# Kernel tuning notes

Measured on AMD Instinct MI355X. Metric: run time of the kernel, lower is better.

## Reference

```python
import jax, jax.numpy as jnp
import numpy as np

N = 50000          # nodes
E = 800000         # edges (before self loops)
H = 4              # attention heads
C = 64             # per-head channels
D_IN = 256
NEG_ATT = 0.2      # GATConv attention LeakyReLU slope
NEG_ACT = 0.01     # nn.LeakyReLU default slope
EPS = 1e-5
MLP_DIMS = [64, 32, 16, 2]


def _gat_layer(x, src, dst, W, a_src, a_dst, b, concat):
    """PyG GATConv: gather -> segment-softmax over dst -> scatter-add."""
    n = x.shape[0]
    h = (x @ W).reshape(n, H, C)                       # [N,H,C]
    s = (h * a_src).sum(-1)                            # [N,H]
    d = (h * a_dst).sum(-1)                            # [N,H]
    e = jax.nn.leaky_relu(s[src] + d[dst], NEG_ATT)    # [E',H]
    m = jax.ops.segment_max(e, dst, num_segments=n)    # per-dst max (self loops -> no empty segs)
    w = jnp.exp(e - m[dst])
    den = jax.ops.segment_sum(w, dst, num_segments=n)
    alpha = w / den[dst]                               # [E',H]
    out = jax.ops.segment_sum(alpha[:, :, None] * h[src], dst, num_segments=n)  # [N,H,C]
    out = out.reshape(n, H * C) if concat else out.mean(axis=1)
    return out + b


def _graph_norm(x, w, b, a):
    mu = x.mean(axis=0, keepdims=True)
    y = x - a * mu
    var = (y * y).mean(axis=0, keepdims=True)
    return w * y * jax.lax.rsqrt(var + EPS) + b


def setup_inputs() -> dict:
    key = jax.random.key(0)
    ks = jax.random.split(key, 40)
    d = {
        'x': jax.random.normal(ks[0], (N, D_IN), dtype=jnp.float32),
        'edge_index': jax.random.randint(ks[1], (2, E), 0, N, dtype=jnp.int64),
    }
    dims_in = [D_IN, H * C, H * C]
    norm_dims = [H * C, H * C, C]
    k = 2
    for i in range(3):
        fan = dims_in[i]
        d[f'W{i}'] = jax.random.normal(ks[k], (fan, H * C), dtype=jnp.float32) / np.sqrt(fan); k += 1
        d[f'as{i}'] = jax.random.normal(ks[k], (H, C), dtype=jnp.float32) / np.sqrt(C); k += 1
        d[f'ad{i}'] = jax.random.normal(ks[k], (H, C), dtype=jnp.float32) / np.sqrt(C); k += 1
        d[f'b{i}'] = jnp.zeros((norm_dims[i],), dtype=jnp.float32)
        d[f'gw{i}'] = jnp.ones((norm_dims[i],), dtype=jnp.float32)
        d[f'gb{i}'] = jnp.zeros((norm_dims[i],), dtype=jnp.float32)
        d[f'ga{i}'] = jnp.ones((norm_dims[i],), dtype=jnp.float32)
    for j in range(3):
        fi, fo = MLP_DIMS[j], MLP_DIMS[j + 1]
        d[f'mW{j}'] = jax.random.normal(ks[k], (fi, fo), dtype=jnp.float32) / np.sqrt(fi); k += 1
        d[f'mb{j}'] = jnp.zeros((fo,), dtype=jnp.float32)
    return d


def reference(x, edge_index,
              W0, as0, ad0, b0, gw0, gb0, ga0,
              W1, as1, ad1, b1, gw1, gb1, ga1,
              W2, as2, ad2, b2, gw2, gb2, ga2,
              mW0, mb0, mW1, mb1, mW2, mb2):
    n = x.shape[0]
    loop = jnp.arange(n, dtype=edge_index.dtype)
    src = jnp.concatenate([edge_index[0], loop])   # add self loops (PyG default)
    dst = jnp.concatenate([edge_index[1], loop])

    h = _gat_layer(x, src, dst, W0, as0, ad0, b0, concat=True)
    h = jax.nn.leaky_relu(_graph_norm(h, gw0, gb0, ga0), NEG_ACT)
    h = _gat_layer(h, src, dst, W1, as1, ad1, b1, concat=True)
    h = jax.nn.leaky_relu(_graph_norm(h, gw1, gb1, ga1), NEG_ACT)
    h = _gat_layer(h, src, dst, W2, as2, ad2, b2, concat=False)
    h = jax.nn.leaky_relu(_graph_norm(h, gw2, gb2, ga2), NEG_ACT)

    h = jax.nn.relu(h @ mW0 + mb0)
    h = jax.nn.relu(h @ mW1 + mb1)
    return h @ mW2 + mb2
```

## Files before the change

kernel.cpp:

```cpp
#include <hip/hip_runtime.h>

#define NN 50000
#define EE 800000
#define ET 850000
#define HH 4
#define CC 64
#define FDIM 256

#define SCAN_BLK 512
#define SCAN_NB ((NN + SCAN_BLK - 1) / SCAN_BLK)

typedef unsigned short ushort;
typedef __bf16 bf16x8 __attribute__((ext_vector_type(8)));
typedef float floatx4 __attribute__((ext_vector_type(4)));
typedef ushort ushort8v __attribute__((ext_vector_type(8)));
struct ushort4s { ushort x, y, z, w; };

__device__ __forceinline__ ushort f2bf(float f) {
  union { float f; unsigned u; } v; v.f = f;
  unsigned r = v.u + 0x7fffu + ((v.u >> 16) & 1u);
  return (ushort)(r >> 16);
}
__device__ __forceinline__ float bf2f(ushort u) {
  return __uint_as_float(((unsigned)u) << 16);
}

__device__ __forceinline__ int get_edge(const void* p, int is64, long long idx) {
  if (is64) return (int)((const long long*)p)[idx];
  return ((const int*)p)[idx];
}

__global__ void detect_kernel(const unsigned int* p, int* flag) {
  __shared__ unsigned red[256];
  int t = threadIdx.x;
  unsigned o = 0;
  for (int i = 0; i < 4; i++) o |= p[(t * 4 + i) * 2 + 1];
  red[t] = o;
  __syncthreads();
  for (int s = 128; s > 0; s >>= 1) {
    if (t < s) red[t] |= red[t + s];
    __syncthreads();
  }
  if (t == 0) *flag = (red[0] == 0) ? 1 : 0;
}

__global__ void degree_kernel(const void* eidx, const int* flag, int* deg) {
  int k = blockIdx.x * blockDim.x + threadIdx.x;
  if (k >= ET) return;
  int is64 = *flag;
  int dst = (k < EE) ? get_edge(eidx, is64, (long long)EE + k) : (k - EE);
  atomicAdd(&deg[dst], 1);
}

__global__ __launch_bounds__(SCAN_BLK) void scan1_kernel(const int* __restrict__ deg,
                                                         int* __restrict__ rowptr,
                                                         int* __restrict__ bsum) {
  __shared__ int sm[SCAN_BLK];
  int t = threadIdx.x;
  int i = blockIdx.x * SCAN_BLK + t;
  int v = (i < NN) ? deg[i] : 0;
  sm[t] = v;
  __syncthreads();
#pragma unroll
  for (int o = 1; o < SCAN_BLK; o <<= 1) {
    int u = (t >= o) ? sm[t - o] : 0;
    __syncthreads();
    sm[t] += u;
    __syncthreads();
  }
  if (i < NN) rowptr[i] = sm[t] - v;
  if (t == SCAN_BLK - 1) bsum[blockIdx.x] = sm[t];
}

__global__ __launch_bounds__(128) void scan2_kernel(const int* __restrict__ bsum,
                                                    int* __restrict__ boff,
                                                    int* __restrict__ rowptr) {
  __shared__ int sm[128];
  int t = threadIdx.x;
  int v = (t < SCAN_NB) ? bsum[t] : 0;
  sm[t] = v;
  __syncthreads();
#pragma unroll
  for (int o = 1; o < 128; o <<= 1) {
    int u = (t >= o) ? sm[t - o] : 0;
    __syncthreads();
    sm[t] += u;
    __syncthreads();
  }
  if (t < SCAN_NB) boff[t] = sm[t] - v;
  if (t == 0) rowptr[NN] = ET;
}

__global__ __launch_bounds__(SCAN_BLK) void scan3_kernel(int* __restrict__ rowptr,
                                                         int* __restrict__ cursor,
                                                         const int* __restrict__ boff) {
  int i = blockIdx.x * SCAN_BLK + threadIdx.x;
  if (i >= NN) return;
  int v = rowptr[i] + boff[blockIdx.x];
  rowptr[i] = v;
  cursor[i] = v;
}

__global__ void fill_kernel(const void* eidx, const int* flag, int* cursor, int* csr_src) {
  int k = blockIdx.x * blockDim.x + threadIdx.x;
  if (k >= ET) return;
  int is64 = *flag;
  int src, dst;
  if (k < EE) {
    src = get_edge(eidx, is64, k);
    dst = get_edge(eidx, is64, (long long)EE + k);
  } else {
    src = dst = k - EE;
  }
  int pos = atomicAdd(&cursor[dst], 1);
  csr_src[pos] = src;
}

__global__ void conv_w_kernel(const float* __restrict__ W0, const float* __restrict__ W1,
                              const float* __restrict__ W2,
                              ushort* __restrict__ T0, ushort* __restrict__ T1,
                              ushort* __restrict__ T2) {
  const float* W = (blockIdx.y == 0) ? W0 : (blockIdx.y == 1) ? W1 : W2;
  ushort* Wt = (blockIdx.y == 0) ? T0 : (blockIdx.y == 1) ? T1 : T2;
  int idx = blockIdx.x * 256 + threadIdx.x;
  int k = idx >> 8, n = idx & 255;
  Wt[n * 256 + k] = f2bf(W[idx]);
}

template <int MODE>
__global__ __launch_bounds__(256) void gemm_bf16(const void* __restrict__ Ap,
                                                 const ushort* __restrict__ Bt,
                                                 ushort* __restrict__ C,
                                                 const float* __restrict__ as_,
                                                 const float* __restrict__ ad_,
                                                 float* __restrict__ s_arr,
                                                 float* __restrict__ d_arr,
                                                 const float* __restrict__ colsum,
                                                 const float* __restrict__ colsumsq,
                                                 const float* __restrict__ ga,
                                                 const float* __restrict__ gw,
                                                 const float* __restrict__ gb) {
  __shared__ ushort As[4 * 512];
  __shared__ ushort Bs[8 * 512];
  __shared__ float scs[FDIM], shs[FDIM];
  int tid = threadIdx.x, w = tid >> 6, l = tid & 63;
  int brow0 = blockIdx.x * 64, bcol0 = blockIdx.y * 128;
  int lm = l & 15, lk = (l >> 4) * 8;
  int arA = min(brow0 + w * 16 + lm, NN - 1);
  size_t arowA = (size_t)arA * 256 + lk;
  const ushort* bg0 = Bt + (size_t)(bcol0 + (2 * w) * 16 + lm) * 256 + lk;
  const ushort* bg1 = Bt + (size_t)(bcol0 + (2 * w + 1) * 16 + lm) * 256 + lk;

  if constexpr (MODE == 1) {
    const float invn = 1.0f / (float)NN;
    float mu = colsum[tid] * invn;
    float ex2 = colsumsq[tid] * invn;
    float a = ga[tid];
    float var = fmaxf(ex2 - (2.f * a - a * a) * mu * mu, 0.f);
    float s = gw[tid] * rsqrtf(var + 1e-5f);
    scs[tid] = s;
    shs[tid] = gb[tid] - s * a * mu;
    __syncthreads();
  }

  floatx4 acc[2][4];
#pragma unroll
  for (int i = 0; i < 2; i++)
#pragma unroll
    for (int j = 0; j < 4; j++) acc[i][j] = floatx4{0.f, 0.f, 0.f, 0.f};

  int wm = (w >> 1) * 2, wn = (w & 1) * 4;

  for (int k0 = 0; k0 < 256; k0 += 32) {
    ushort8v a0;
    if constexpr (MODE == 0) {
      const float* p0 = (const float*)Ap + arowA + k0;
      float4 u0 = *(const float4*)p0, v0 = *(const float4*)(p0 + 4);
      a0 = ushort8v{f2bf(u0.x), f2bf(u0.y), f2bf(u0.z), f2bf(u0.w),
                    f2bf(v0.x), f2bf(v0.y), f2bf(v0.z), f2bf(v0.w)};
    } else {
      ushort8v r0 = *(const ushort8v*)((const ushort*)Ap + arowA + k0);
      int kb = k0 + lk;
#pragma unroll
      for (int j = 0; j < 8; j++) {
        float sc = scs[kb + j], sh = shs[kb + j];
        float y0 = fmaf(sc, bf2f(r0[j]), sh);
        y0 = fmaxf(y0, 0.01f * y0);
        a0[j] = f2bf(y0);
      }
    }
    ushort8v b0 = *(const ushort8v*)(bg0 + k0);
    ushort8v b1 = *(const ushort8v*)(bg1 + k0);
    *(ushort8v*)&As[w * 512 + l * 8] = a0;
    *(ushort8v*)&Bs[(2 * w) * 512 + l * 8] = b0;
    *(ushort8v*)&Bs[(2 * w + 1) * 512 + l * 8] = b1;
    __syncthreads();
    bf16x8 af[2], bfr[4];
#pragma unroll
    for (int i = 0; i < 2; i++) af[i] = *(const bf16x8*)&As[(wm + i) * 512 + l * 8];
#pragma unroll
    for (int j = 0; j < 4; j++) bfr[j] = *(const bf16x8*)&Bs[(wn + j) * 512 + l * 8];
#pragma unroll
    for (int i = 0; i < 2; i++)
#pragma unroll
      for (int j = 0; j < 4; j++)
        acc[i][j] = __builtin_amdgcn_mfma_f32_16x16x32_bf16(af[i], bfr[j], acc[i][j], 0, 0, 0);
    __syncthreads();
  }

  int quad = l >> 4;
#pragma unroll
  for (int i = 0; i < 2; i++) {
    int r0 = brow0 + (wm + i) * 16 + quad * 4;
#pragma unroll
    for (int j = 0; j < 4; j++) {
      int col = bcol0 + (wn + j) * 16 + lm;
#pragma unroll
      for (int r = 0; r < 4; r++) {
        int row = r0 + r;
        if (row < NN) C[(size_t)row * 256 + col] = f2bf(acc[i][j][r]);
      }
    }
  }
  float asv[4], adv[4];
#pragma unroll
  for (int j = 0; j < 4; j++) {
    int col = bcol0 + (wn + j) * 16 + lm;
    asv[j] = as_[col];
    adv[j] = ad_[col];
  }
  int head = (bcol0 >> 6) + (w & 1);
#pragma unroll
  for (int i = 0; i < 2; i++) {
#pragma unroll
    for (int r = 0; r < 4; r++) {
      float sp = acc[i][0][r] * asv[0] + acc[i][1][r] * asv[1] +
                 acc[i][2][r] * asv[2] + acc[i][3][r] * asv[3];
      float dp = acc[i][0][r] * adv[0] + acc[i][1][r] * adv[1] +
                 acc[i][2][r] * adv[2] + acc[i][3][r] * adv[3];
      sp += __shfl_xor(sp, 1); dp += __shfl_xor(dp, 1);
      sp += __shfl_xor(sp, 2); dp += __shfl_xor(dp, 2);
      sp += __shfl_xor(sp, 4); dp += __shfl_xor(dp, 4);
      sp += __shfl_xor(sp, 8); dp += __shfl_xor(dp, 8);
      if (lm == 0) {
        int row = brow0 + (wm + i) * 16 + quad * 4 + r;
        if (row < NN) {
          s_arr[row * HH + head] = sp;
          d_arr[row * HH + head] = dp;
        }
      }
    }
  }
}

template <bool CONCAT>
__global__ __launch_bounds__(256) void agg_kernel(const ushort* __restrict__ hb,
                                                  const float* __restrict__ s_arr,
                                                  const float* __restrict__ d_arr,
                                                  const int* __restrict__ rowptr,
                                                  const int* __restrict__ csr_src,
                                                  const float* __restrict__ bias,
                                                  void* __restrict__ outp) {
  int w = __builtin_amdgcn_readfirstlane(threadIdx.x >> 6);
  int l = threadIdx.x & 63;
  int head = l >> 4;
  int n = blockIdx.x * 4 + w;
  int beg = rowptr[n], end = rowptr[n + 1];
  float dh = d_arr[n * HH + head];
  float a0 = 0.f, a1 = 0.f, a2 = 0.f, a3 = 0.f, den = 0.f;

  int i = beg;
  for (; i + 16 <= end; i += 16) {
    int ss[16];
#pragma unroll
    for (int t = 0; t < 16; t++) ss[t] = csr_src[i + t];
    float ee[16];
#pragma unroll
    for (int t = 0; t < 16; t++) ee[t] = s_arr[ss[t] * HH + head];
    ushort4s hh[16];
#pragma unroll
    for (int t = 0; t < 16; t++)
      hh[t] = *(const ushort4s*)(hb + (unsigned)(ss[t] * FDIM + l * 4));
#pragma unroll
    for (int t = 0; t < 16; t++) {
      float e = ee[t] + dh;
      e = (e > 0.f) ? e : 0.2f * e;
      float wt = __expf(e);
      den += wt;
      a0 = fmaf(wt, bf2f(hh[t].x), a0);
      a1 = fmaf(wt, bf2f(hh[t].y), a1);
      a2 = fmaf(wt, bf2f(hh[t].z), a2);
      a3 = fmaf(wt, bf2f(hh[t].w), a3);
    }
  }
  for (; i + 8 <= end; i += 8) {
    int ss[8];
#pragma unroll
    for (int t = 0; t < 8; t++) ss[t] = csr_src[i + t];
    float ee[8];
#pragma unroll
    for (int t = 0; t < 8; t++) ee[t] = s_arr[ss[t] * HH + head];
    ushort4s hh[8];
#pragma unroll
    for (int t = 0; t < 8; t++)
      hh[t] = *(const ushort4s*)(hb + (unsigned)(ss[t] * FDIM + l * 4));
#pragma unroll
    for (int t = 0; t < 8; t++) {
      float e = ee[t] + dh;
      e = (e > 0.f) ? e : 0.2f * e;
      float wt = __expf(e);
      den += wt;
      a0 = fmaf(wt, bf2f(hh[t].x), a0);
      a1 = fmaf(wt, bf2f(hh[t].y), a1);
      a2 = fmaf(wt, bf2f(hh[t].z), a2);
      a3 = fmaf(wt, bf2f(hh[t].w), a3);
    }
  }
  for (; i + 4 <= end; i += 4) {
    int ss[4];
#pragma unroll
    for (int t = 0; t < 4; t++) ss[t] = csr_src[i + t];
    float ee[4];
#pragma unroll
    for (int t = 0; t < 4; t++) ee[t] = s_arr[ss[t] * HH + head];
    ushort4s hh[4];
#pragma unroll
    for (int t = 0; t < 4; t++)
      hh[t] = *(const ushort4s*)(hb + (unsigned)(ss[t] * FDIM + l * 4));
#pragma unroll
    for (int t = 0; t < 4; t++) {
      float e = ee[t] + dh;
      e = (e > 0.f) ? e : 0.2f * e;
      float wt = __expf(e);
      den += wt;
      a0 = fmaf(wt, bf2f(hh[t].x), a0);
      a1 = fmaf(wt, bf2f(hh[t].y), a1);
      a2 = fmaf(wt, bf2f(hh[t].z), a2);
      a3 = fmaf(wt, bf2f(hh[t].w), a3);
    }
  }
  for (; i < end; i++) {
    int s0 = csr_src[i];
    float e0 = s_arr[s0 * HH + head] + dh;
    ushort4s h0 = *(const ushort4s*)(hb + (unsigned)(s0 * FDIM + l * 4));
    e0 = (e0 > 0.f) ? e0 : 0.2f * e0;
    float w0 = __expf(e0);
    den += w0;
    a0 = fmaf(w0, bf2f(h0.x), a0); a1 = fmaf(w0, bf2f(h0.y), a1);
    a2 = fmaf(w0, bf2f(h0.z), a2); a3 = fmaf(w0, bf2f(h0.w), a3);
  }
  float inv = 1.0f / den;
  float r0 = a0 * inv, r1 = a1 * inv, r2 = a2 * inv, r3 = a3 * inv;

  if (CONCAT) {
    float4 bv = ((const float4*)bias)[l];
    ushort4s o;
    o.x = f2bf(r0 + bv.x); o.y = f2bf(r1 + bv.y);
    o.z = f2bf(r2 + bv.z); o.w = f2bf(r3 + bv.w);
    ((ushort4s*)outp)[(unsigned)(n * 64 + l)] = o;
  } else {
    r0 += __shfl_xor(r0, 16); r1 += __shfl_xor(r1, 16);
    r2 += __shfl_xor(r2, 16); r3 += __shfl_xor(r3, 16);
    r0 += __shfl_xor(r0, 32); r1 += __shfl_xor(r1, 32);
    r2 += __shfl_xor(r2, 32); r3 += __shfl_xor(r3, 32);
    if (l < 16) {
      float4 bv = ((const float4*)bias)[l];
      float4 o;
      o.x = 0.25f * r0 + bv.x; o.y = 0.25f * r1 + bv.y;
      o.z = 0.25f * r2 + bv.z; o.w = 0.25f * r3 + bv.w;
      ((float4*)outp)[(unsigned)(n * 16 + l)] = o;
    }
  }
}

__global__ __launch_bounds__(256) void norm_reduce_bf(const ushort* __restrict__ xin,
                                                      float* colsum, float* colsumsq) {
  __shared__ float4 sm1[256], sm2[256];
  int t = threadIdx.x;
  int c4 = (t & 63) * 4;
  int rl = t >> 6;
  int r0 = blockIdx.x * 128;
  int r1 = min(NN, r0 + 128);
  float s0 = 0.f, s1 = 0.f, s2 = 0.f, s3 = 0.f;
  float q0 = 0.f, q1 = 0.f, q2 = 0.f, q3 = 0.f;
  for (int r = r0 + rl; r < r1; r += 4) {
    ushort4s v = *(const ushort4s*)(xin + (size_t)r * FDIM + c4);
    float f0 = bf2f(v.x), f1 = bf2f(v.y), f2 = bf2f(v.z), f3 = bf2f(v.w);
    s0 += f0; q0 += f0 * f0;
    s1 += f1; q1 += f1 * f1;
    s2 += f2; q2 += f2 * f2;
    s3 += f3; q3 += f3 * f3;
  }
  sm1[t] = float4{s0, s1, s2, s3};
  sm2[t] = float4{q0, q1, q2, q3};
  __syncthreads();
  if (t < 64) {
    float4 a = sm1[t], b = sm1[t + 64], c = sm1[t + 128], d = sm1[t + 192];
    atomicAdd(&colsum[c4 + 0], a.x + b.x + c.x + d.x);
    atomicAdd(&colsum[c4 + 1], a.y + b.y + c.y + d.y);
    atomicAdd(&colsum[c4 + 2], a.z + b.z + c.z + d.z);
    atomicAdd(&colsum[c4 + 3], a.w + b.w + c.w + d.w);
    float4 e = sm2[t], f = sm2[t + 64], g = sm2[t + 128], h = sm2[t + 192];
    atomicAdd(&colsumsq[c4 + 0], e.x + f.x + g.x + h.x);
    atomicAdd(&colsumsq[c4 + 1], e.y + f.y + g.y + h.y);
    atomicAdd(&colsumsq[c4 + 2], e.z + f.z + g.z + h.z);
    atomicAdd(&colsumsq[c4 + 3], e.w + f.w + g.w + h.w);
  }
}

__global__ __launch_bounds__(256) void norm_reduce_f32(const float* __restrict__ xin,
                                                       float* colsum, float* colsumsq) {
  int f = threadIdx.x & (CC - 1);
  int rl = threadIdx.x / CC;
  int r0 = blockIdx.x * 128;
  int r1 = min(NN, r0 + 128);
  float s1 = 0.f, s2 = 0.f;
  for (int r = r0 + rl; r < r1; r += 4) {
    float v = xin[(size_t)r * CC + f];
    s1 += v; s2 += v * v;
  }
  atomicAdd(&colsum[f], s1);
  atomicAdd(&colsumsq[f], s2);
}

__global__ __launch_bounds__(256) void mlp_kernel(const float* __restrict__ xin,
                                                  const float* __restrict__ colsum,
                                                  const float* __restrict__ colsumsq,
                                                  const float* __restrict__ ga,
                                                  const float* __restrict__ gw,
                                                  const float* __restrict__ gb,
                                                  const float* mW0, const float* mb0,
                                                  const float* mW1, const float* mb1,
                                                  const float* mW2, const float* mb2,
                                                  float* __restrict__ out) {
  __shared__ float W0s[64 * 32];
  __shared__ float W1s[32 * 16];
  __shared__ float W2s[16 * 2];
  __shared__ float b0s[32], b1s[16], b2s[2];
  __shared__ float sc[CC], sh[CC];
  int t = threadIdx.x;
  for (int i = t; i < 2048; i += 256) W0s[i] = mW0[i];
  for (int i = t; i < 512; i += 256) W1s[i] = mW1[i];
  if (t < 32) { W2s[t] = mW2[t]; b0s[t] = mb0[t]; }
  if (t < 16) b1s[t] = mb1[t];
  if (t < 2) b2s[t] = mb2[t];
  if (t < CC) {
    const float invn = 1.0f / (float)NN;
    float mu = colsum[t] * invn;
    float ex2 = colsumsq[t] * invn;
    float a = ga[t];
    float var = fmaxf(ex2 - (2.f * a - a * a) * mu * mu, 0.f);
    float s = gw[t] * rsqrtf(var + 1e-5f);
    sc[t] = s; sh[t] = gb[t] - s * a * mu;
  }
  __syncthreads();
  int node = blockIdx.x * 256 + t;
  if (node >= NN) return;
  float in[64];
  const float* xr = xin + (size_t)node * 64;
#pragma unroll
  for (int k = 0; k < 64; k++) {
    float y = sc[k] * xr[k] + sh[k];
    in[k] = (y > 0.f) ? y : 0.01f * y;
  }
  float h1[32];
#pragma unroll
  for (int j = 0; j < 32; j++) h1[j] = b0s[j];
#pragma unroll
  for (int k = 0; k < 64; k++) {
    float v = in[k];
#pragma unroll
    for (int j = 0; j < 32; j++) h1[j] += v * W0s[k * 32 + j];
  }
#pragma unroll
  for (int j = 0; j < 32; j++) h1[j] = fmaxf(h1[j], 0.f);
  float h2[16];
#pragma unroll
  for (int j = 0; j < 16; j++) h2[j] = b1s[j];
#pragma unroll
  for (int k = 0; k < 32; k++) {
    float v = h1[k];
#pragma unroll
    for (int j = 0; j < 16; j++) h2[j] += v * W1s[k * 16 + j];
  }
#pragma unroll
  for (int j = 0; j < 16; j++) h2[j] = fmaxf(h2[j], 0.f);
  float o0 = b2s[0], o1 = b2s[1];
#pragma unroll
  for (int k = 0; k < 16; k++) {
    o0 += h2[k] * W2s[k * 2 + 0];
    o1 += h2[k] * W2s[k * 2 + 1];
  }
  out[(size_t)node * 2 + 0] = o0;
  out[(size_t)node * 2 + 1] = o1;
}

extern "C" void kernel_launch(void* const* d_in, const int* in_sizes, int n_in,
                              void* d_out, int out_size, void* d_ws, size_t ws_size,
                              hipStream_t stream) {
  const float* x = (const float*)d_in[0];
  const void* ei = d_in[1];
  const float* W[3]   = {(const float*)d_in[2],  (const float*)d_in[9],  (const float*)d_in[16]};
  const float* as_[3] = {(const float*)d_in[3],  (const float*)d_in[10], (const float*)d_in[17]};
  const float* ad_[3] = {(const float*)d_in[4],  (const float*)d_in[11], (const float*)d_in[18]};
  const float* b_[3]  = {(const float*)d_in[5],  (const float*)d_in[12], (const float*)d_in[19]};
  const float* gw[3]  = {(const float*)d_in[6],  (const float*)d_in[13], (const float*)d_in[20]};
  const float* gb[3]  = {(const float*)d_in[7],  (const float*)d_in[14], (const float*)d_in[21]};
  const float* ga[3]  = {(const float*)d_in[8],  (const float*)d_in[15], (const float*)d_in[22]};
  const float* mW0 = (const float*)d_in[23];
  const float* mb0 = (const float*)d_in[24];
  const float* mW1 = (const float*)d_in[25];
  const float* mb1 = (const float*)d_in[26];
  const float* mW2 = (const float*)d_in[27];
  const float* mb2 = (const float*)d_in[28];
  float* out = (float*)d_out;

  char* ws = (char*)d_ws;
  size_t off = 0;
  auto take = [&](size_t bytes) -> char* {
    char* p = ws + off;
    off = (off + bytes + 255) & ~(size_t)255;
    return p;
  };
  ushort* hb    = (ushort*)take((size_t)NN * FDIM * 2);
  ushort* aggb  = (ushort*)take((size_t)NN * FDIM * 2);
  float* bufD   = (float*)take((size_t)NN * CC * 4);
  ushort* Wt[3];
  for (int i = 0; i < 3; i++) Wt[i] = (ushort*)take((size_t)256 * 256 * 2);
  float* s_arr  = (float*)take((size_t)NN * HH * 4);
  float* d_arr  = (float*)take((size_t)NN * HH * 4);
  char* zbase   = (char*)take(0);
  int* deg      = (int*)take((size_t)NN * 4);
  float* cs[3];
  for (int i = 0; i < 3; i++) cs[i] = (float*)take(2048);
  size_t zlen   = (size_t)(((char*)cs[2] + 2048) - zbase);
  int* cursor   = (int*)take((size_t)NN * 4);
  int* rowptr   = (int*)take((size_t)(NN + 1) * 4);
  int* csr_src  = (int*)take((size_t)ET * 4);
  int* bsum     = (int*)take(512);
  int* boff     = (int*)take(512);
  int* flag     = (int*)take(256);

  hipMemsetAsync(zbase, 0, zlen, stream);

  detect_kernel<<<1, 256, 0, stream>>>((const unsigned int*)ei, flag);
  degree_kernel<<<(ET + 255) / 256, 256, 0, stream>>>(ei, flag, deg);
  scan1_kernel<<<SCAN_NB, SCAN_BLK, 0, stream>>>(deg, rowptr, bsum);
  scan2_kernel<<<1, 128, 0, stream>>>(bsum, boff, rowptr);
  scan3_kernel<<<SCAN_NB, SCAN_BLK, 0, stream>>>(rowptr, cursor, boff);
  fill_kernel<<<(ET + 255) / 256, 256, 0, stream>>>(ei, flag, cursor, csr_src);

  conv_w_kernel<<<dim3(256, 3), 256, 0, stream>>>(W[0], W[1], W[2], Wt[0], Wt[1], Wt[2]);

  dim3 ggrid((NN + 63) / 64, 2);
  for (int L = 0; L < 3; L++) {
    if (L == 0)
      gemm_bf16<0><<<ggrid, 256, 0, stream>>>((const void*)x, Wt[0], hb,
                                              as_[0], ad_[0], s_arr, d_arr,
                                              nullptr, nullptr, nullptr, nullptr, nullptr);
    else
      gemm_bf16<1><<<ggrid, 256, 0, stream>>>((const void*)aggb, Wt[L], hb,
                                              as_[L], ad_[L], s_arr, d_arr,
                                              cs[L - 1], cs[L - 1] + 256,
                                              ga[L - 1], gw[L - 1], gb[L - 1]);
    if (L < 2) {
      agg_kernel<true><<<NN / 4, 256, 0, stream>>>(hb, s_arr, d_arr, rowptr, csr_src, b_[L], aggb);
      norm_reduce_bf<<<(NN + 127) / 128, 256, 0, stream>>>(aggb, cs[L], cs[L] + 256);
    } else {
      agg_kernel<false><<<NN / 4, 256, 0, stream>>>(hb, s_arr, d_arr, rowptr, csr_src, b_[L], bufD);
      norm_reduce_f32<<<(NN + 127) / 128, 256, 0, stream>>>(bufD, cs[2], cs[2] + 256);
    }
  }
  mlp_kernel<<<(NN + 255) / 256, 256, 0, stream>>>(bufD, cs[2], cs[2] + 256,
                                                   ga[2], gw[2], gb[2],
                                                   mW0, mb0, mW1, mb1, mW2, mb2, out);
}
```

Measured before the change: 686.2 us.

## Retile GEMM to full-width 32-row blocks and detect int64 edges on host

The GEMM block now covers 32 rows and all 256 output columns, with each wave owning one head of 64 columns, instead of a 64x128 tile over a 2D grid. Each A row is therefore loaded and, in mode 1, normalised and converted only once rather than once per column block, and each head's attention dot products come from a single wave. The price is that every block reloads the whole B matrix, and there are more blocks. The device-side index-dtype detection kernel is also removed and replaced by a host check on the input byte size, which drops one launch and a dependent flag read.

New measurement: 705.1 us. 2.8% more time.

```diff
diff --git a/kernel.cpp b/kernel.cpp
--- a/kernel.cpp
+++ b/kernel.cpp
@@ -14,6 +14,7 @@
 typedef __bf16 bf16x8 __attribute__((ext_vector_type(8)));
 typedef float floatx4 __attribute__((ext_vector_type(4)));
 typedef ushort ushort8v __attribute__((ext_vector_type(8)));
+typedef ushort ushort4v __attribute__((ext_vector_type(4)));
 struct ushort4s { ushort x, y, z, w; };
 
 __device__ __forceinline__ ushort f2bf(float f) {
@@ -30,24 +31,9 @@
   return ((const int*)p)[idx];
 }
 
-__global__ void detect_kernel(const unsigned int* p, int* flag) {
-  __shared__ unsigned red[256];
-  int t = threadIdx.x;
-  unsigned o = 0;
-  for (int i = 0; i < 4; i++) o |= p[(t * 4 + i) * 2 + 1];
-  red[t] = o;
-  __syncthreads();
-  for (int s = 128; s > 0; s >>= 1) {
-    if (t < s) red[t] |= red[t + s];
-    __syncthreads();
-  }
-  if (t == 0) *flag = (red[0] == 0) ? 1 : 0;
-}
-
-__global__ void degree_kernel(const void* eidx, const int* flag, int* deg) {
+__global__ void degree_kernel(const void* eidx, int is64, int* deg) {
   int k = blockIdx.x * blockDim.x + threadIdx.x;
   if (k >= ET) return;
-  int is64 = *flag;
   int dst = (k < EE) ? get_edge(eidx, is64, (long long)EE + k) : (k - EE);
   atomicAdd(&deg[dst], 1);
 }
@@ -101,10 +87,9 @@
   cursor[i] = v;
 }
 
-__global__ void fill_kernel(const void* eidx, const int* flag, int* cursor, int* csr_src) {
+__global__ void fill_kernel(const void* eidx, int is64, int* cursor, int* csr_src) {
   int k = blockIdx.x * blockDim.x + threadIdx.x;
   if (k >= ET) return;
-  int is64 = *flag;
   int src, dst;
   if (k < EE) {
     src = get_edge(eidx, is64, k);
@@ -140,16 +125,23 @@
                                                  const float* __restrict__ ga,
                                                  const float* __restrict__ gw,
                                                  const float* __restrict__ gb) {
-  __shared__ ushort As[4 * 512];
-  __shared__ ushort Bs[8 * 512];
+  __shared__ ushort As[2 * 512];
+  __shared__ ushort Bs[16 * 512];
   __shared__ float scs[FDIM], shs[FDIM];
   int tid = threadIdx.x, w = tid >> 6, l = tid & 63;
-  int brow0 = blockIdx.x * 64, bcol0 = blockIdx.y * 128;
+  int brow0 = blockIdx.x * 32;
   int lm = l & 15, lk = (l >> 4) * 8;
-  int arA = min(brow0 + w * 16 + lm, NN - 1);
-  size_t arowA = (size_t)arA * 256 + lk;
-  const ushort* bg0 = Bt + (size_t)(bcol0 + (2 * w) * 16 + lm) * 256 + lk;
-  const ushort* bg1 = Bt + (size_t)(bcol0 + (2 * w + 1) * 16 + lm) * 256 + lk;
+  int s_sub = tid >> 7;
+  int within = tid & 127;
+  int arow = brow0 + s_sub * 16 + ((within >> 1) & 15);
+  arow = min(arow, NN - 1);
+  int kbase = ((within >> 5) << 3) + ((within & 1) << 2);
+  size_t aoff = (size_t)arow * 256 + kbase;
+  int aldst = s_sub * 512 + within * 4;
+  const ushort* bg[4];
+#pragma unroll
+  for (int j = 0; j < 4; j++)
+    bg[j] = Bt + (size_t)((4 * w + j) * 16 + lm) * 256 + lk;
 
   if constexpr (MODE == 1) {
     const float invn = 1.0f / (float)NN;
@@ -169,37 +161,36 @@
 #pragma unroll
     for (int j = 0; j < 4; j++) acc[i][j] = floatx4{0.f, 0.f, 0.f, 0.f};
 
-  int wm = (w >> 1) * 2, wn = (w & 1) * 4;
-
   for (int k0 = 0; k0 < 256; k0 += 32) {
-    ushort8v a0;
+    ushort4v av;
     if constexpr (MODE == 0) {
-      const float* p0 = (const float*)Ap + arowA + k0;
-      float4 u0 = *(const float4*)p0, v0 = *(const float4*)(p0 + 4);
-      a0 = ushort8v{f2bf(u0.x), f2bf(u0.y), f2bf(u0.z), f2bf(u0.w),
-                    f2bf(v0.x), f2bf(v0.y), f2bf(v0.z), f2bf(v0.w)};
+      float4 u = *(const float4*)((const float*)Ap + aoff + k0);
+      av = ushort4v{f2bf(u.x), f2bf(u.y), f2bf(u.z), f2bf(u.w)};
     } else {
-      ushort8v r0 = *(const ushort8v*)((const ushort*)Ap + arowA + k0);
-      int kb = k0 + lk;
-#pragma unroll
-      for (int j = 0; j < 8; j++) {
-        float sc = scs[kb + j], sh = shs[kb + j];
-        float y0 = fmaf(sc, bf2f(r0[j]), sh);
-        y0 = fmaxf(y0, 0.01f * y0);
-        a0[j] = f2bf(y0);
+      ushort4v r = *(const ushort4v*)((const ushort*)Ap + aoff + k0);
+      int kb = k0 + kbase;
+#pragma unroll
+      for (int j = 0; j < 4; j++) {
+        float y = fmaf(scs[kb + j], bf2f(r[j]), shs[kb + j]);
+        y = fmaxf(y, 0.01f * y);
+        av[j] = f2bf(y);
       }
     }
-    ushort8v b0 = *(const ushort8v*)(bg0 + k0);
-    ushort8v b1 = *(const ushort8v*)(bg1 + k0);
-    *(ushort8v*)&As[w * 512 + l * 8] = a0;
-    *(ushort8v*)&Bs[(2 * w) * 512 + l * 8] = b0;
-    *(ushort8v*)&Bs[(2 * w + 1) * 512 + l * 8] = b1;
+    ushort8v b0 = *(const ushort8v*)(bg[0] + k0);
+    ushort8v b1 = *(const ushort8v*)(bg[1] + k0);
+    ushort8v b2 = *(const ushort8v*)(bg[2] + k0);
+    ushort8v b3 = *(const ushort8v*)(bg[3] + k0);
+    *(ushort4v*)&As[aldst] = av;
+    *(ushort8v*)&Bs[(4 * w + 0) * 512 + l * 8] = b0;
+    *(ushort8v*)&Bs[(4 * w + 1) * 512 + l * 8] = b1;
+    *(ushort8v*)&Bs[(4 * w + 2) * 512 + l * 8] = b2;
+    *(ushort8v*)&Bs[(4 * w + 3) * 512 + l * 8] = b3;
     __syncthreads();
     bf16x8 af[2], bfr[4];
-#pragma unroll
-    for (int i = 0; i < 2; i++) af[i] = *(const bf16x8*)&As[(wm + i) * 512 + l * 8];
-#pragma unroll
-    for (int j = 0; j < 4; j++) bfr[j] = *(const bf16x8*)&Bs[(wn + j) * 512 + l * 8];
+    af[0] = *(const bf16x8*)&As[l * 8];
+    af[1] = *(const bf16x8*)&As[512 + l * 8];
+#pragma unroll
+    for (int j = 0; j < 4; j++) bfr[j] = *(const bf16x8*)&Bs[(4 * w + j) * 512 + l * 8];
 #pragma unroll
     for (int i = 0; i < 2; i++)
 #pragma unroll
@@ -211,13 +202,13 @@
   int quad = l >> 4;
 #pragma unroll
   for (int i = 0; i < 2; i++) {
-    int r0 = brow0 + (wm + i) * 16 + quad * 4;
+    int rr0 = brow0 + i * 16 + quad * 4;
 #pragma unroll
     for (int j = 0; j < 4; j++) {
-      int col = bcol0 + (wn + j) * 16 + lm;
+      int col = w * 64 + j * 16 + lm;
 #pragma unroll
       for (int r = 0; r < 4; r++) {
-        int row = r0 + r;
+        int row = rr0 + r;
         if (row < NN) C[(size_t)row * 256 + col] = f2bf(acc[i][j][r]);
       }
     }
@@ -225,11 +216,10 @@
   float asv[4], adv[4];
 #pragma unroll
   for (int j = 0; j < 4; j++) {
-    int col = bcol0 + (wn + j) * 16 + lm;
+    int col = w * 64 + j * 16 + lm;
     asv[j] = as_[col];
     adv[j] = ad_[col];
   }
-  int head = (bcol0 >> 6) + (w & 1);
 #pragma unroll
   for (int i = 0; i < 2; i++) {
 #pragma unroll
@@ -243,10 +233,10 @@
       sp += __shfl_xor(sp, 4); dp += __shfl_xor(dp, 4);
       sp += __shfl_xor(sp, 8); dp += __shfl_xor(dp, 8);
       if (lm == 0) {
-        int row = brow0 + (wm + i) * 16 + quad * 4 + r;
+        int row = brow0 + i * 16 + quad * 4 + r;
         if (row < NN) {
-          s_arr[row * HH + head] = sp;
-          d_arr[row * HH + head] = dp;
+          s_arr[row * HH + w] = sp;
+          d_arr[row * HH + w] = dp;
         }
       }
     }
@@ -515,6 +505,8 @@
   const float* mb2 = (const float*)d_in[28];
   float* out = (float*)d_out;
 
+  int is64 = (in_sizes[1] == (int)(2u * EE * 8u)) ? 1 : 0;
+
   char* ws = (char*)d_ws;
   size_t off = 0;
   auto take = [&](size_t bytes) -> char* {
@@ -539,20 +531,18 @@
   int* csr_src  = (int*)take((size_t)ET * 4);
   int* bsum     = (int*)take(512);
   int* boff     = (int*)take(512);
-  int* flag     = (int*)take(256);
 
   hipMemsetAsync(zbase, 0, zlen, stream);
 
-  detect_kernel<<<1, 256, 0, stream>>>((const unsigned int*)ei, flag);
-  degree_kernel<<<(ET + 255) / 256, 256, 0, stream>>>(ei, flag, deg);
+  degree_kernel<<<(ET + 255) / 256, 256, 0, stream>>>(ei, is64, deg);
   scan1_kernel<<<SCAN_NB, SCAN_BLK, 0, stream>>>(deg, rowptr, bsum);
   scan2_kernel<<<1, 128, 0, stream>>>(bsum, boff, rowptr);
   scan3_kernel<<<SCAN_NB, SCAN_BLK, 0, stream>>>(rowptr, cursor, boff);
-  fill_kernel<<<(ET + 255) / 256, 256, 0, stream>>>(ei, flag, cursor, csr_src);
+  fill_kernel<<<(ET + 255) / 256, 256, 0, stream>>>(ei, is64, cursor, csr_src);
 
   conv_w_kernel<<<dim3(256, 3), 256, 0, stream>>>(W[0], W[1], W[2], Wt[0], Wt[1], Wt[2]);
 
-  dim3 ggrid((NN + 63) / 64, 2);
+  int ggrid = (NN + 31) / 32;
   for (int L = 0; L < 3; L++) {
     if (L == 0)
       gemm_bf16<0><<<ggrid, 256, 0, stream>>>((const void*)x, Wt[0], hb,
```

## Double-buffer GEMM tiles via direct global-to-LDS loads and pre-convert x to bf16

Applied to the files above, without the earlier changes.

The GEMM now stages A and B tiles with global_load_lds into double-buffered shared memory, prefetching the next K slice while the current one is consumed. This halves the barriers per iteration and hides load latency. The normalization and activation transform for layers 1 and 2 moves to after the LDS read. The layer-0 input x is converted to bf16 by a separate kernel, and the detect kernel is replaced by a host-side size check on edge_index. The cost is an extra pass over x and an extra workspace buffer, and the new code relies on LDS-direct load ordering being correct with a single barrier per stage.

Result: no change. 692.3 us (+0.9%).

```diff
diff --git a/kernel.cpp b/kernel.cpp
--- a/kernel.cpp
+++ b/kernel.cpp
@@ -25,29 +25,20 @@
   return __uint_as_float(((unsigned)u) << 16);
 }
 
+__device__ __forceinline__ void gload16(const void* gsrc, void* ldst) {
+  __builtin_amdgcn_global_load_lds(
+      (const __attribute__((address_space(1))) void*)gsrc,
+      (__attribute__((address_space(3))) void*)ldst, 16, 0, 0);
+}
+
 __device__ __forceinline__ int get_edge(const void* p, int is64, long long idx) {
   if (is64) return (int)((const long long*)p)[idx];
   return ((const int*)p)[idx];
 }
 
-__global__ void detect_kernel(const unsigned int* p, int* flag) {
-  __shared__ unsigned red[256];
-  int t = threadIdx.x;
-  unsigned o = 0;
-  for (int i = 0; i < 4; i++) o |= p[(t * 4 + i) * 2 + 1];
-  red[t] = o;
-  __syncthreads();
-  for (int s = 128; s > 0; s >>= 1) {
-    if (t < s) red[t] |= red[t + s];
-    __syncthreads();
-  }
-  if (t == 0) *flag = (red[0] == 0) ? 1 : 0;
-}
-
-__global__ void degree_kernel(const void* eidx, const int* flag, int* deg) {
+__global__ void degree_kernel(const void* eidx, int is64, int* deg) {
   int k = blockIdx.x * blockDim.x + threadIdx.x;
   if (k >= ET) return;
-  int is64 = *flag;
   int dst = (k < EE) ? get_edge(eidx, is64, (long long)EE + k) : (k - EE);
   atomicAdd(&deg[dst], 1);
 }
@@ -101,10 +92,9 @@
   cursor[i] = v;
 }
 
-__global__ void fill_kernel(const void* eidx, const int* flag, int* cursor, int* csr_src) {
+__global__ void fill_kernel(const void* eidx, int is64, int* cursor, int* csr_src) {
   int k = blockIdx.x * blockDim.x + threadIdx.x;
   if (k >= ET) return;
-  int is64 = *flag;
   int src, dst;
   if (k < EE) {
     src = get_edge(eidx, is64, k);
@@ -127,8 +117,18 @@
   Wt[n * 256 + k] = f2bf(W[idx]);
 }
 
+__global__ __launch_bounds__(256) void cvt_x_kernel(const float* __restrict__ x,
+                                                    ushort* __restrict__ xb) {
+  int i = blockIdx.x * 256 + threadIdx.x;
+  const float4* p = (const float4*)x + (size_t)i * 2;
+  float4 a = p[0], b = p[1];
+  ushort8v o{f2bf(a.x), f2bf(a.y), f2bf(a.z), f2bf(a.w),
+             f2bf(b.x), f2bf(b.y), f2bf(b.z), f2bf(b.w)};
+  *(ushort8v*)(xb + (size_t)i * 8) = o;
+}
+
 template <int MODE>
-__global__ __launch_bounds__(256) void gemm_bf16(const void* __restrict__ Ap,
+__global__ __launch_bounds__(256) void gemm_bf16(const ushort* __restrict__ Abf,
                                                  const ushort* __restrict__ Bt,
                                                  ushort* __restrict__ C,
                                                  const float* __restrict__ as_,
@@ -140,16 +140,19 @@
                                                  const float* __restrict__ ga,
                                                  const float* __restrict__ gw,
                                                  const float* __restrict__ gb) {
-  __shared__ ushort As[4 * 512];
-  __shared__ ushort Bs[8 * 512];
+  __shared__ ushort As[2][4][512];
+  __shared__ ushort Bs[2][8][512];
   __shared__ float scs[FDIM], shs[FDIM];
   int tid = threadIdx.x, w = tid >> 6, l = tid & 63;
   int brow0 = blockIdx.x * 64, bcol0 = blockIdx.y * 128;
   int lm = l & 15, lk = (l >> 4) * 8;
-  int arA = min(brow0 + w * 16 + lm, NN - 1);
-  size_t arowA = (size_t)arA * 256 + lk;
+  int arow = min(brow0 + w * 16 + lm, NN - 1);
+  const ushort* ag  = Abf + (size_t)arow * 256 + lk;
   const ushort* bg0 = Bt + (size_t)(bcol0 + (2 * w) * 16 + lm) * 256 + lk;
   const ushort* bg1 = Bt + (size_t)(bcol0 + (2 * w + 1) * 16 + lm) * 256 + lk;
+  ushort* lA  = &As[0][w][l * 8];
+  ushort* lB0 = &Bs[0][2 * w][l * 8];
+  ushort* lB1 = &Bs[0][2 * w + 1][l * 8];
 
   if constexpr (MODE == 1) {
     const float invn = 1.0f / (float)NN;
@@ -160,64 +163,77 @@
     float s = gw[tid] * rsqrtf(var + 1e-5f);
     scs[tid] = s;
     shs[tid] = gb[tid] - s * a * mu;
+  }
+
+  gload16(ag, lA);
+  gload16(bg0, lB0);
+  gload16(bg1, lB1);
+
+  floatx4 acc[2][4];
+#pragma unroll
+  for (int i = 0; i < 2; i++)
+#pragma unroll
+    for (int j = 0; j < 4; j++) acc[i][j] = floatx4{0.f, 0.f, 0.f, 0.f};
+
+  int wm = (w >> 1) * 2, wn = (w & 1) * 4;
+
+#pragma unroll
+  for (int s = 0; s < 8; ++s) {
+    int buf = s & 1;
     __syncthreads();
-  }
-
-  floatx4 acc[2][4];
-#pragma unroll
-  for (int i = 0; i < 2; i++)
-#pragma unroll
-    for (int j = 0; j < 4; j++) acc[i][j] = floatx4{0.f, 0.f, 0.f, 0.f};
-
-  int wm = (w >> 1) * 2, wn = (w & 1) * 4;
-
-  for (int k0 = 0; k0 < 256; k0 += 32) {
-    ushort8v a0;
+    if (s < 7) {
+      int k1 = (s + 1) * 32;
+      int ao = (buf ^ 1) * 2048;
+      int bo = (buf ^ 1) * 4096;
+      gload16(ag + k1, lA + ao);
+      gload16(bg0 + k1, lB0 + bo);
+      gload16(bg1 + k1, lB1 + bo);
+    }
+    bf16x8 af[2], bfr[4];
     if constexpr (MODE == 0) {
-      const float* p0 = (const float*)Ap + arowA + k0;
-      float4 u0 = *(const float4*)p0, v0 = *(const float4*)(p0 + 4);
-      a0 = ushort8v{f2bf(u0.x), f2bf(u0.y), f2bf(u0.z), f2bf(u0.w),
-                    f2bf(v0.x), f2bf(v0.y), f2bf(v0.z), f2bf(v0.w)};
+#pragma unroll
+      for (int i = 0; i < 2; i++) af[i] = *(const bf16x8*)&As[buf][wm + i][l * 8];
     } else {
-      ushort8v r0 = *(const ushort8v*)((const ushort*)Ap + arowA + k0);
-      int kb = k0 + lk;
-#pragma unroll
-      for (int j = 0; j < 8; j++) {
-        float sc = scs[kb + j], sh = shs[kb + j];
-        float y0 = fmaf(sc, bf2f(r0[j]), sh);
-        y0 = fmaxf(y0, 0.01f * y0);
-        a0[j] = f2bf(y0);
+      int k = s * 32 + lk;
+      float4 sc0 = *(const float4*)&scs[k];
+      float4 sc1 = *(const float4*)&scs[k + 4];
+      float4 sh0 = *(const float4*)&shs[k];
+      float4 sh1 = *(const float4*)&shs[k + 4];
+#pragma unroll
+      for (int i = 0; i < 2; i++) {
+        ushort8v r = *(const ushort8v*)&As[buf][wm + i][l * 8];
+        ushort8v a;
+#pragma unroll
+        for (int j = 0; j < 4; j++) {
+          float y0 = fmaf(((const float*)&sc0)[j], bf2f(r[j]), ((const float*)&sh0)[j]);
+          float y1 = fmaf(((const float*)&sc1)[j], bf2f(r[j + 4]), ((const float*)&sh1)[j]);
+          y0 = fmaxf(y0, 0.01f * y0);
+          y1 = fmaxf(y1, 0.01f * y1);
+          a[j] = f2bf(y0);
+          a[j + 4] = f2bf(y1);
+        }
+        af[i] = *(bf16x8*)&a;
       }
     }
-    ushort8v b0 = *(const ushort8v*)(bg0 + k0);
-    ushort8v b1 = *(const ushort8v*)(bg1 + k0);
-    *(ushort8v*)&As[w * 512 + l * 8] = a0;
-    *(ushort8v*)&Bs[(2 * w) * 512 + l * 8] = b0;
-    *(ushort8v*)&Bs[(2 * w + 1) * 512 + l * 8] = b1;
-    __syncthreads();
-    bf16x8 af[2], bfr[4];
-#pragma unroll
-    for (int i = 0; i < 2; i++) af[i] = *(const bf16x8*)&As[(wm + i) * 512 + l * 8];
-#pragma unroll
-    for (int j = 0; j < 4; j++) bfr[j] = *(const bf16x8*)&Bs[(wn + j) * 512 + l * 8];
+#pragma unroll
+    for (int j = 0; j < 4; j++) bfr[j] = *(const bf16x8*)&Bs[buf][wn + j][l * 8];
 #pragma unroll
     for (int i = 0; i < 2; i++)
 #pragma unroll
       for (int j = 0; j < 4; j++)
         acc[i][j] = __builtin_amdgcn_mfma_f32_16x16x32_bf16(af[i], bfr[j], acc[i][j], 0, 0, 0);
-    __syncthreads();
   }
 
   int quad = l >> 4;
 #pragma unroll
   for (int i = 0; i < 2; i++) {
-    int r0 = brow0 + (wm + i) * 16 + quad * 4;
+    int rr0 = brow0 + (wm + i) * 16 + quad * 4;
 #pragma unroll
     for (int j = 0; j < 4; j++) {
       int col = bcol0 + (wn + j) * 16 + lm;
 #pragma unroll
       for (int r = 0; r < 4; r++) {
-        int row = r0 + r;
+        int row = rr0 + r;
         if (row < NN) C[(size_t)row * 256 + col] = f2bf(acc[i][j][r]);
       }
     }
@@ -515,6 +531,8 @@
   const float* mb2 = (const float*)d_in[28];
   float* out = (float*)d_out;
 
+  int is64 = (in_sizes[1] == (int)(2u * EE * 8u)) ? 1 : 0;
+
   char* ws = (char*)d_ws;
   size_t off = 0;
   auto take = [&](size_t bytes) -> char* {
@@ -524,6 +542,7 @@
   };
   ushort* hb    = (ushort*)take((size_t)NN * FDIM * 2);
   ushort* aggb  = (ushort*)take((size_t)NN * FDIM * 2);
+  ushort* xbf   = (ushort*)take((size_t)NN * FDIM * 2);
   float* bufD   = (float*)take((size_t)NN * CC * 4);
   ushort* Wt[3];
   for (int i = 0; i < 3; i++) Wt[i] = (ushort*)take((size_t)256 * 256 * 2);
@@ -539,27 +558,26 @@
   int* csr_src  = (int*)take((size_t)ET * 4);
   int* bsum     = (int*)take(512);
   int* boff     = (int*)take(512);
-  int* flag     = (int*)take(256);
 
   hipMemsetAsync(zbase, 0, zlen, stream);
 
-  detect_kernel<<<1, 256, 0, stream>>>((const unsigned int*)ei, flag);
-  degree_kernel<<<(ET + 255) / 256, 256, 0, stream>>>(ei, flag, deg);
+  degree_kernel<<<(ET + 255) / 256, 256, 0, stream>>>(ei, is64, deg);
   scan1_kernel<<<SCAN_NB, SCAN_BLK, 0, stream>>>(deg, rowptr, bsum);
   scan2_kernel<<<1, 128, 0, stream>>>(bsum, boff, rowptr);
   scan3_kernel<<<SCAN_NB, SCAN_BLK, 0, stream>>>(rowptr, cursor, boff);
-  fill_kernel<<<(ET + 255) / 256, 256, 0, stream>>>(ei, flag, cursor, csr_src);
+  fill_kernel<<<(ET + 255) / 256, 256, 0, stream>>>(ei, is64, cursor, csr_src);
 
   conv_w_kernel<<<dim3(256, 3), 256, 0, stream>>>(W[0], W[1], W[2], Wt[0], Wt[1], Wt[2]);
+  cvt_x_kernel<<<(NN * FDIM / 8 + 255) / 256, 256, 0, stream>>>(x, xbf);
 
   dim3 ggrid((NN + 63) / 64, 2);
   for (int L = 0; L < 3; L++) {
     if (L == 0)
-      gemm_bf16<0><<<ggrid, 256, 0, stream>>>((const void*)x, Wt[0], hb,
+      gemm_bf16<0><<<ggrid, 256, 0, stream>>>(xbf, Wt[0], hb,
                                               as_[0], ad_[0], s_arr, d_arr,
                                               nullptr, nullptr, nullptr, nullptr, nullptr);
     else
-      gemm_bf16<1><<<ggrid, 256, 0, stream>>>((const void*)aggb, Wt[L], hb,
+      gemm_bf16<1><<<ggrid, 256, 0, stream>>>(aggb, Wt[L], hb,
                                               as_[L], ad_[L], s_arr, d_arr,
                                               cs[L - 1], cs[L - 1] + 256,
                                               ga[L - 1], gw[L - 1], gb[L - 1]);
```
